# Kernel tuning notes

Measured on AMD Instinct MI355X. Metric: run time of the kernel, lower is better.

## Reference

```python
import jax, jax.numpy as jnp
import numpy as np

N_NODES = 50000


def _relgraphconv(x, W, Wloop, b, src, dst, etypes, n_nodes):
    # DGL RelGraphConv (regularizer=None, self_loop=True, norm=None):
    # out[i] = sum over incoming edges (j->i, rel r) of W_r @ x[j]  +  W_loop @ x[i]  +  b
    # low-mem form: transform all nodes per relation, then gather per edge.
    h_rel = jnp.einsum('ni,rio->rno', x, W)          # [R, N, out]
    msg = h_rel[etypes, src]                          # [E, out]
    agg = jax.ops.segment_sum(msg, dst, num_segments=n_nodes)  # [N, out]
    return agg + x @ Wloop + b


def setup_inputs() -> dict:
    key = jax.random.key(0)
    ks = jax.random.split(key, 12)
    N, E, n_state = N_NODES, 800000, 128
    inp = {
        'x': jax.random.normal(ks[0], (N, n_state), dtype=jnp.float32),
        'src': jax.random.randint(ks[1], (E,), 0, N, dtype=jnp.int32),
        'dst': jax.random.randint(ks[2], (E,), 0, N, dtype=jnp.int32),
        'etypes': jax.random.randint(ks[3], (E,), 0, 2, dtype=jnp.int32),
        'cell_size': jax.random.randint(ks[4], (N,), 0, 8, dtype=jnp.int32),
        'max_size': jax.random.randint(ks[5], (N,), 0, 8, dtype=jnp.int32),
        'W1': jax.random.normal(ks[6], (2, n_state, 64), dtype=jnp.float32) * 0.05,
        'loop1': jax.random.normal(ks[7], (n_state, 64), dtype=jnp.float32) * 0.05,
        'b1': jnp.zeros((64,), dtype=jnp.float32),
        'W2': jax.random.normal(ks[8], (2, 64, 64), dtype=jnp.float32) * 0.05,
        'loop2': jax.random.normal(ks[9], (64, 64), dtype=jnp.float32) * 0.05,
        'b2': jnp.zeros((64,), dtype=jnp.float32),
        'W3': jax.random.normal(ks[10], (2, 64, 2), dtype=jnp.float32) * 0.05,
        'loop3': jax.random.normal(ks[11], (64, 2), dtype=jnp.float32) * 0.05,
        'b3': jnp.zeros((2,), dtype=jnp.float32),
    }
    return inp


def reference(x, src, dst, etypes, cell_size, max_size,
              W1, loop1, b1, W2, loop2, b2, W3, loop3, b3):
    N = x.shape[0]
    h = jax.nn.relu(_relgraphconv(x, W1, loop1, b1, src, dst, etypes, N))
    h = jax.nn.relu(_relgraphconv(h, W2, loop2, b2, src, dst, etypes, N))
    h = _relgraphconv(h, W3, loop3, b3, src, dst, etypes, N)   # [N, 2]
    # action mask: col 0 = cannot upsize, col 1 = cannot downsize
    upper = cell_size >= (max_size - 1)
    lower = cell_size == 0
    mask = jnp.stack([upper, lower], axis=1)                   # [N, 2] bool
    return jnp.where(mask, h.min() - 1.0, h)
```

## Files before the change

### kernel.cpp

```cpp
#include <hip/hip_runtime.h>


#define STRIDE 64
#define BINCAP 2560

typedef unsigned short ushortT;
typedef __attribute__((ext_vector_type(8))) short short8;
typedef __attribute__((ext_vector_type(4))) float f32x4;

__device__ inline ushortT f2bf(float f) {
    union { float f; unsigned u; } v; v.f = f;
    unsigned r = v.u + 0x7FFFu + ((v.u >> 16) & 1u);
    return (ushortT)(r >> 16);
}
__device__ inline float bf2f(ushortT h) {
    union { unsigned u; float f; } v; v.u = ((unsigned)h) << 16;
    return v.f;
}

__device__ inline void atomicMinF(float* addr, float v) {
    if (v >= 0.f) atomicMin((int*)addr, __float_as_int(v));
    else          atomicMax((unsigned int*)addr, __float_as_uint(v));
}

__global__ __launch_bounds__(256) void pack_init_kernel(
    const float* __restrict__ W1, const float* __restrict__ loop1,
    const float* __restrict__ W2, const float* __restrict__ loop2,
    ushortT* __restrict__ BP1, ushortT* __restrict__ BP2,
    int* __restrict__ bincnt, float* __restrict__ minval, int NBINS) {
    int g = (int)blockIdx.x * 256 + (int)threadIdx.x;
    if (g < NBINS) bincnt[g] = 0;
    if (g == 0) *(int*)minval = 0x7f7f7f7f;
    if (g < 3072) {
        int l = g & 63, ks = (g >> 6) & 3, ct = g >> 8;
        int c = ct * 16 + (l & 15);
        int mat = c >> 6, cc = c & 63;
        int kbase = ks * 32 + (l >> 4) * 8;
        ushortT* dstp = BP1 + (size_t)g * 8;
#pragma unroll
        for (int j = 0; j < 8; ++j) {
            int k = kbase + j;
            float v = (mat < 2) ? W1[((size_t)mat * 128 + k) * 64 + cc]
                                : loop1[(size_t)k * 64 + cc];
            dstp[j] = f2bf(v);
        }
    } else {
        int s = g - 3072;
        int l = s & 63;
        int ks = (s >> 6) % 6;
        int ct = s / 384;
        int c = ct * 16 + (l & 15);
        int kbase = ks * 32 + (l >> 4) * 8;
        ushortT* dstp = BP2 + (size_t)s * 8;
#pragma unroll
        for (int j = 0; j < 8; ++j) {
            int k = kbase + j;
            float v = (k < 128) ? W2[(size_t)k * 64 + c]
                                : loop2[(size_t)(k - 128) * 64 + c];
            dstp[j] = f2bf(v);
        }
    }
}

__global__ __launch_bounds__(256) void k1_kernel(
    const float* __restrict__ x, const ushortT* __restrict__ BP1,
    const float* __restrict__ b1,
    ushortT* __restrict__ hrelb, ushortT* __restrict__ H1b,
    const int* __restrict__ src, const int* __restrict__ dst,
    const int* __restrict__ et, int* __restrict__ bincnt, int2* __restrict__ binbuf,
    int N, int E, int NBINS, int NBA) {
    __shared__ int hist[512];
    __shared__ int gbase[512];
    __shared__ ushortT rnk[4096];

    const int t = (int)threadIdx.x;

    if ((int)blockIdx.x < NBA) {
        for (int i = t; i < NBINS; i += 256) hist[i] = 0;
        __syncthreads();
        const int base = (int)blockIdx.x * 4096;
#pragma unroll
        for (int i = 0; i < 16; ++i) {
            int e = base + t + i * 256;
            if (e < E) {
                int bb = dst[e] >> 7;
                rnk[t + i * 256] = (ushortT)atomicAdd(&hist[bb], 1);
            }
        }
        __syncthreads();
        for (int i = t; i < NBINS; i += 256) {
            int h = hist[i];
            gbase[i] = h ? atomicAdd(&bincnt[i], h) : 0;
        }
        __syncthreads();
#pragma unroll
        for (int i = 0; i < 16; ++i) {
            int e = base + t + i * 256;
            if (e < E) {
                int dd = dst[e];
                int bb = dd >> 7;
                int v = et[e] * N + src[e];
                int pos = gbase[bb] + (int)rnk[t + i * 256];
                if (pos < BINCAP)
                    binbuf[(size_t)bb * BINCAP + pos] = make_int2(dd, v);
            }
        }
        return;
    }
    const int w = t >> 6, lane = t & 63;
    const int rowbase = (((int)blockIdx.x - NBA) * 4 + w) * 16;
    const int m = lane & 15, quad = lane >> 4;
    const int nclamp = min(rowbase + m, N - 1);

    short8 a[4];
    const float* xp = x + (size_t)nclamp * 128 + quad * 8;
#pragma unroll
    for (int ks = 0; ks < 4; ++ks) {
        float4 g0 = *(const float4*)(xp + ks * 32);
        float4 g1 = *(const float4*)(xp + ks * 32 + 4);
        a[ks][0] = (short)f2bf(g0.x); a[ks][1] = (short)f2bf(g0.y);
        a[ks][2] = (short)f2bf(g0.z); a[ks][3] = (short)f2bf(g0.w);
        a[ks][4] = (short)f2bf(g1.x); a[ks][5] = (short)f2bf(g1.y);
        a[ks][6] = (short)f2bf(g1.z); a[ks][7] = (short)f2bf(g1.w);
    }

    f32x4 acc[12];
#pragma unroll
    for (int ct = 0; ct < 12; ++ct) acc[ct] = (f32x4){0.f, 0.f, 0.f, 0.f};

#pragma unroll
    for (int ks = 0; ks < 4; ++ks) {
#pragma unroll
        for (int ct = 0; ct < 12; ++ct) {
            short8 b = *(const short8*)&BP1[((size_t)(ct * 4 + ks) * 64 + lane) * 8];
            acc[ct] = __builtin_amdgcn_mfma_f32_16x16x32_bf16(a[ks], b, acc[ct], 0, 0, 0);
        }
    }

    const int node0 = rowbase + quad * 4;
#pragma unroll
    for (int ct = 0; ct < 12; ++ct) {
        int c = ct * 16 + m;
        int mat = c >> 6, cc = c & 63;
        float bias = (mat == 2) ? b1[cc] : 0.f;
#pragma unroll
        for (int j = 0; j < 4; ++j) {
            int n = node0 + j;
            if (n < N) {
                float v = acc[ct][j] + bias;
                if (mat < 2) hrelb[((size_t)mat * N + n) * 64 + cc] = f2bf(v);
                else         H1b[(size_t)n * 64 + cc] = f2bf(v);
            }
        }
    }
}

__global__ __launch_bounds__(256) void phaseB_kernel(
    const int* __restrict__ bincnt, const int2* __restrict__ binbuf,
    int* __restrict__ cnt, int* __restrict__ eidx, int N) {
    __shared__ int lcnt[128];
    const int b = (int)blockIdx.x;
    const int t = (int)threadIdx.x;
    if (t < 128) lcnt[t] = 0;
    __syncthreads();
    const int cb = min(bincnt[b], BINCAP);
    const int2* buf = binbuf + (size_t)b * BINCAP;
    for (int i = t; i < cb; i += 256) {
        int2 rec = buf[i];
        int r = atomicAdd(&lcnt[rec.x & 127], 1);
        if (r < STRIDE) eidx[(size_t)rec.x * STRIDE + r] = rec.y;
    }
    __syncthreads();
    int node = b * 128 + t;
    if (t < 128 && node < N) cnt[node] = min(lcnt[t], STRIDE);
}

__device__ __forceinline__ float gather_accum(
    const ushortT* __restrict__ hb, int my, int deg, int lane, float acc) {
    for (int j = 0; j < deg; j += 16) {
        float v[16];
#pragma unroll
        for (int q = 0; q < 16; ++q) {
            int jj = j + q;
            int sel = (jj < deg) ? jj : 0;
            int id = __shfl(my, sel, 64);
            float wgt = (jj < deg) ? 1.f : 0.f;
            v[q] = wgt * bf2f(hb[(size_t)id * 64 + lane]);
        }
        float s0 = (v[0] + v[1]) + (v[2] + v[3]);
        float s1 = (v[4] + v[5]) + (v[6] + v[7]);
        float s2 = (v[8] + v[9]) + (v[10] + v[11]);
        float s3 = (v[12] + v[13]) + (v[14] + v[15]);
        acc += (s0 + s1) + (s2 + s3);
    }
    return acc;
}

__global__ void agg1_kernel(const ushortT* __restrict__ hrelb, const int* __restrict__ eidx,
                            const int* __restrict__ cnt, ushortT* __restrict__ H1b, int N) {
    int node = (int)blockIdx.x * 4 + ((int)threadIdx.x >> 6);
    if (node >= N) return;
    int lane = (int)threadIdx.x & 63;
    int deg = cnt[node];
    int my = (lane < deg) ? eidx[(size_t)node * STRIDE + lane] : 0;
    float acc = bf2f(H1b[(size_t)node * 64 + lane]);
    acc = gather_accum(hrelb, my, deg, lane, acc);
    H1b[(size_t)node * 64 + lane] = f2bf(fmaxf(acc, 0.f));
}

__global__ void agg2_kernel(const ushortT* __restrict__ H1b, const int* __restrict__ eidx,
                            const int* __restrict__ cnt, ushortT* __restrict__ Sb, int N) {
    int node = (int)blockIdx.x * 4 + ((int)threadIdx.x >> 6);
    if (node >= N) return;
    int lane = (int)threadIdx.x & 63;
    int deg = cnt[node];
    int my = (lane < deg) ? eidx[(size_t)node * STRIDE + lane] : 0;
    float a0 = 0.f, a1 = 0.f;
    for (int j = 0; j < deg; j += 16) {
        float v[16], w0[16], w1[16];
#pragma unroll
        for (int q = 0; q < 16; ++q) {
            int jj = j + q;
            int sel = (jj < deg) ? jj : 0;
            int id = __shfl(my, sel, 64);
            int rel = (id >= N) ? 1 : 0;
            int row = id - rel * N;
            float live = (jj < deg) ? 1.f : 0.f;
            w0[q] = rel ? 0.f : live;
            w1[q] = rel ? live : 0.f;
            v[q] = bf2f(H1b[(size_t)row * 64 + lane]);
        }
#pragma unroll
        for (int q = 0; q < 16; ++q) {
            a0 += w0[q] * v[q];
            a1 += w1[q] * v[q];
        }
    }
    Sb[(size_t)node * 64 + lane] = f2bf(a0);
    Sb[((size_t)N + node) * 64 + lane] = f2bf(a1);
}

__global__ __launch_bounds__(256) void gemm23_kernel(
    const ushortT* __restrict__ Sb, const ushortT* __restrict__ H1b,
    const ushortT* __restrict__ BP2, const float* __restrict__ b2,
    const float* __restrict__ W3, const float* __restrict__ loop3,
    const float* __restrict__ b3,
    float* __restrict__ hrel3, float* __restrict__ H3, int N) {
    const int w = (int)threadIdx.x >> 6, lane = (int)threadIdx.x & 63;
    const int rowbase = ((int)blockIdx.x * 4 + w) * 16;
    const int m = lane & 15, quad = lane >> 4;
    const int nclamp = min(rowbase + m, N - 1);

    f32x4 acc[4];
#pragma unroll
    for (int ct = 0; ct < 4; ++ct) acc[ct] = (f32x4){0.f, 0.f, 0.f, 0.f};

#pragma unroll
    for (int ks = 0; ks < 6; ++ks) {
        const ushortT* base =
            (ks < 2) ? (Sb + (size_t)nclamp * 64)
          : (ks < 4) ? (Sb + ((size_t)N + nclamp) * 64)
                     : (H1b + (size_t)nclamp * 64);
        short8 a = *(const short8*)(base + (ks & 1) * 32 + quad * 8);
#pragma unroll
        for (int ct = 0; ct < 4; ++ct) {
            short8 b = *(const short8*)&BP2[((size_t)(ct * 6 + ks) * 64 + lane) * 8];
            acc[ct] = __builtin_amdgcn_mfma_f32_16x16x32_bf16(a, b, acc[ct], 0, 0, 0);
        }
    }

    float h2[4][4];
#pragma unroll
    for (int ct = 0; ct < 4; ++ct) {
        float bias = b2[ct * 16 + m];
#pragma unroll
        for (int j = 0; j < 4; ++j) h2[ct][j] = fmaxf(acc[ct][j] + bias, 0.f);
    }

    float w3v[4][6];
#pragma unroll
    for (int ct = 0; ct < 4; ++ct) {
        int k = ct * 16 + m;
        w3v[ct][0] = W3[k * 2 + 0];
        w3v[ct][1] = W3[k * 2 + 1];
        w3v[ct][2] = W3[(64 + k) * 2 + 0];
        w3v[ct][3] = W3[(64 + k) * 2 + 1];
        w3v[ct][4] = loop3[k * 2 + 0];
        w3v[ct][5] = loop3[k * 2 + 1];
    }
    float p[4][6];
#pragma unroll
    for (int j = 0; j < 4; ++j)
#pragma unroll
        for (int c = 0; c < 6; ++c) p[j][c] = 0.f;
#pragma unroll
    for (int j = 0; j < 4; ++j)
#pragma unroll
        for (int ct = 0; ct < 4; ++ct)
#pragma unroll
            for (int c = 0; c < 6; ++c) p[j][c] += h2[ct][j] * w3v[ct][c];

#pragma unroll
    for (int mask = 1; mask <= 8; mask <<= 1) {
#pragma unroll
        for (int j = 0; j < 4; ++j)
#pragma unroll
            for (int c = 0; c < 6; ++c) p[j][c] += __shfl_xor(p[j][c], mask, 64);
    }

    if (m == 0) {
#pragma unroll
        for (int j = 0; j < 4; ++j) {
            int n = rowbase + quad * 4 + j;
            if (n < N) {
                hrel3[(size_t)n * 2 + 0] = p[j][0];
                hrel3[(size_t)n * 2 + 1] = p[j][1];
                hrel3[((size_t)N + n) * 2 + 0] = p[j][2];
                hrel3[((size_t)N + n) * 2 + 1] = p[j][3];
                H3[(size_t)n * 2 + 0] = p[j][4] + b3[0];
                H3[(size_t)n * 2 + 1] = p[j][5] + b3[1];
            }
        }
    }
}

__global__ void agg3min_kernel(const float* __restrict__ hrel3, const int* __restrict__ eidx,
                               const int* __restrict__ cnt, float* __restrict__ H3,
                               float* __restrict__ minval, int N) {
    int n = (int)blockIdx.x * 256 + (int)threadIdx.x;
    float v = 3.4e38f;
    if (n < N) {
        float a0 = H3[n * 2 + 0], a1 = H3[n * 2 + 1];
        int deg = cnt[n];
        const int* row = &eidx[(size_t)n * STRIDE];
        for (int j = 0; j < deg; j += 8) {
            float2 q[8];
            float wg[8];
#pragma unroll
            for (int qq = 0; qq < 8; ++qq) {
                int jj = j + qq;
                int sel = (jj < deg) ? jj : 0;
                int idx = row[sel];
                wg[qq] = (jj < deg) ? 1.f : 0.f;
                q[qq] = *(const float2*)&hrel3[(size_t)idx * 2];
            }
#pragma unroll
            for (int qq = 0; qq < 8; ++qq) {
                a0 += wg[qq] * q[qq].x;
                a1 += wg[qq] * q[qq].y;
            }
        }
        H3[n * 2 + 0] = a0;
        H3[n * 2 + 1] = a1;
        v = fminf(a0, a1);
    }
#pragma unroll
    for (int mm = 32; mm >= 1; mm >>= 1) v = fminf(v, __shfl_xor(v, mm, 64));
    __shared__ float s[4];
    if ((threadIdx.x & 63) == 0) s[threadIdx.x >> 6] = v;
    __syncthreads();
    if (threadIdx.x == 0)
        atomicMinF(minval, fminf(fminf(s[0], s[1]), fminf(s[2], s[3])));
}

__global__ void mask_kernel(const float* __restrict__ H3, const float* __restrict__ minval,
                            const int* __restrict__ cs, const int* __restrict__ ms,
                            float* __restrict__ out, int N) {
    int n = (int)blockIdx.x * 256 + (int)threadIdx.x;
    if (n >= N) return;
    float m = minval[0] - 1.0f;
    bool up = cs[n] >= ms[n] - 1;
    bool lo = cs[n] == 0;
    out[n * 2 + 0] = up ? m : H3[n * 2 + 0];
    out[n * 2 + 1] = lo ? m : H3[n * 2 + 1];
}

extern "C" void kernel_launch(void* const* d_in, const int* in_sizes, int n_in,
                              void* d_out, int out_size, void* d_ws, size_t ws_size,
                              hipStream_t stream) {
    const float* x     = (const float*)d_in[0];
    const int* src     = (const int*)d_in[1];
    const int* dst     = (const int*)d_in[2];
    const int* etypes  = (const int*)d_in[3];
    const int* cellsz  = (const int*)d_in[4];
    const int* maxsz   = (const int*)d_in[5];
    const float* W1    = (const float*)d_in[6];
    const float* loop1 = (const float*)d_in[7];
    const float* b1    = (const float*)d_in[8];
    const float* W2    = (const float*)d_in[9];
    const float* loop2 = (const float*)d_in[10];
    const float* b2    = (const float*)d_in[11];
    const float* W3    = (const float*)d_in[12];
    const float* loop3 = (const float*)d_in[13];
    const float* b3    = (const float*)d_in[14];
    float* out = (float*)d_out;

    const int N = in_sizes[0] / 128;
    const int E = in_sizes[1];

    char* p = (char*)d_ws;
    auto alloc = [&](size_t bytes) -> void* {
        void* r = (void*)p;
        p += ((bytes + 255) / 256) * 256;
        return r;
    };
    ushortT* hrelb  = (ushortT*)alloc((size_t)2 * N * 64 * 2);
    ushortT* H1b    = (ushortT*)alloc((size_t)N * 64 * 2);
    ushortT* Sb     = (ushortT*)alloc((size_t)2 * N * 64 * 2);
    float* hrel3    = (float*)alloc((size_t)2 * N * 2 * 4);
    float* H3       = (float*)alloc((size_t)N * 2 * 4);
    int* cnt        = (int*)alloc((size_t)N * 4);
    int* eidx       = (int*)alloc((size_t)N * STRIDE * 4);
    ushortT* BP1    = (ushortT*)alloc((size_t)3072 * 8 * 2);
    ushortT* BP2    = (ushortT*)alloc((size_t)1536 * 8 * 2);
    float* minval   = (float*)alloc(4);

    const int NBINS = (N + 127) >> 7;
    int* bincnt     = (int*)alloc((size_t)NBINS * 4);
    int2* binbuf    = (int2*)alloc((size_t)NBINS * BINCAP * 8);
    (void)ws_size; (void)n_in; (void)out_size;

    const int NB_N   = (N + 255) / 256;
    const int NTILES = (N + 63) / 64;
    const int NB_W   = (N + 3) / 4;
    const int NBA    = (E + 4095) / 4096;

    pack_init_kernel<<<18, 256, 0, stream>>>(
        W1, loop1, W2, loop2, BP1, BP2, bincnt, minval, NBINS);

    k1_kernel<<<NBA + NTILES, 256, 0, stream>>>(
        x, BP1, b1, hrelb, H1b,
        src, dst, etypes, bincnt, binbuf, N, E, NBINS, NBA);

    phaseB_kernel<<<NBINS, 256, 0, stream>>>(bincnt, binbuf, cnt, eidx, N);

    agg1_kernel<<<NB_W, 256, 0, stream>>>(hrelb, eidx, cnt, H1b, N);

    agg2_kernel<<<NB_W, 256, 0, stream>>>(H1b, eidx, cnt, Sb, N);

    gemm23_kernel<<<NTILES, 256, 0, stream>>>(Sb, H1b, BP2, b2, W3, loop3, b3,
                                              hrel3, H3, N);

    agg3min_kernel<<<NB_N, 256, 0, stream>>>(hrel3, eidx, cnt, H3, minval, N);
    mask_kernel<<<NB_N, 256, 0, stream>>>(H3, minval, cellsz, maxsz, out, N);
}
```

Before: 218.6 us.

## Regroup prologue kernels: fuse weight packing with binning, GEMM1 with bin scatter

Reorganizes the first three launches. Weight packing now shares a launch with edge binning (phase A), and the layer-1 GEMM shares a launch with the per-node scatter of binned edges (phase B), using a block-index split in each. The bincnt zeroing moves to a hipMemsetAsync. This cuts one kernel launch and lets the independent GEMM work overlap the phase-B scatter. The cost is an extra memset call, and phase-B blocks now carry the GEMM kernel's register footprint.

```diff
diff --git a/kernel.cpp b/kernel.cpp
--- a/kernel.cpp
+++ b/kernel.cpp
@@ -23,92 +23,112 @@
     else          atomicMax((unsigned int*)addr, __float_as_uint(v));
 }
 
-__global__ __launch_bounds__(256) void pack_init_kernel(
+__global__ __launch_bounds__(256) void pack_phaseA_kernel(
     const float* __restrict__ W1, const float* __restrict__ loop1,
     const float* __restrict__ W2, const float* __restrict__ loop2,
     ushortT* __restrict__ BP1, ushortT* __restrict__ BP2,
-    int* __restrict__ bincnt, float* __restrict__ minval, int NBINS) {
-    int g = (int)blockIdx.x * 256 + (int)threadIdx.x;
-    if (g < NBINS) bincnt[g] = 0;
-    if (g == 0) *(int*)minval = 0x7f7f7f7f;
-    if (g < 3072) {
-        int l = g & 63, ks = (g >> 6) & 3, ct = g >> 8;
-        int c = ct * 16 + (l & 15);
-        int mat = c >> 6, cc = c & 63;
-        int kbase = ks * 32 + (l >> 4) * 8;
-        ushortT* dstp = BP1 + (size_t)g * 8;
-#pragma unroll
-        for (int j = 0; j < 8; ++j) {
-            int k = kbase + j;
-            float v = (mat < 2) ? W1[((size_t)mat * 128 + k) * 64 + cc]
-                                : loop1[(size_t)k * 64 + cc];
-            dstp[j] = f2bf(v);
-        }
-    } else {
-        int s = g - 3072;
-        int l = s & 63;
-        int ks = (s >> 6) % 6;
-        int ct = s / 384;
-        int c = ct * 16 + (l & 15);
-        int kbase = ks * 32 + (l >> 4) * 8;
-        ushortT* dstp = BP2 + (size_t)s * 8;
-#pragma unroll
-        for (int j = 0; j < 8; ++j) {
-            int k = kbase + j;
-            float v = (k < 128) ? W2[(size_t)k * 64 + c]
-                                : loop2[(size_t)(k - 128) * 64 + c];
-            dstp[j] = f2bf(v);
-        }
-    }
-}
-
-__global__ __launch_bounds__(256) void k1_kernel(
+    float* __restrict__ minval,
+    const int* __restrict__ src, const int* __restrict__ dst,
+    const int* __restrict__ et, int* __restrict__ bincnt, int2* __restrict__ binbuf,
+    int N, int E, int NBINS) {
+    __shared__ int hist[512];
+    __shared__ int gbase[512];
+    __shared__ ushortT rnk[4096];
+    const int t = (int)threadIdx.x;
+
+    if ((int)blockIdx.x < 18) {
+        int g = (int)blockIdx.x * 256 + t;
+        if (g == 0) *(int*)minval = 0x7f7f7f7f;
+        if (g < 3072) {
+            int l = g & 63, ks = (g >> 6) & 3, ct = g >> 8;
+            int c = ct * 16 + (l & 15);
+            int mat = c >> 6, cc = c & 63;
+            int kbase = ks * 32 + (l >> 4) * 8;
+            ushortT* dstp = BP1 + (size_t)g * 8;
+#pragma unroll
+            for (int j = 0; j < 8; ++j) {
+                int k = kbase + j;
+                float v = (mat < 2) ? W1[((size_t)mat * 128 + k) * 64 + cc]
+                                    : loop1[(size_t)k * 64 + cc];
+                dstp[j] = f2bf(v);
+            }
+        } else {
+            int s = g - 3072;
+            int l = s & 63;
+            int ks = (s >> 6) % 6;
+            int ct = s / 384;
+            int c = ct * 16 + (l & 15);
+            int kbase = ks * 32 + (l >> 4) * 8;
+            ushortT* dstp = BP2 + (size_t)s * 8;
+#pragma unroll
+            for (int j = 0; j < 8; ++j) {
+                int k = kbase + j;
+                float v = (k < 128) ? W2[(size_t)k * 64 + c]
+                                    : loop2[(size_t)(k - 128) * 64 + c];
+                dstp[j] = f2bf(v);
+            }
+        }
+        return;
+    }
+    for (int i = t; i < NBINS; i += 256) hist[i] = 0;
+    __syncthreads();
+    const int base = ((int)blockIdx.x - 18) * 4096;
+#pragma unroll
+    for (int i = 0; i < 16; ++i) {
+        int e = base + t + i * 256;
+        if (e < E) {
+            int bb = dst[e] >> 7;
+            rnk[t + i * 256] = (ushortT)atomicAdd(&hist[bb], 1);
+        }
+    }
+    __syncthreads();
+    for (int i = t; i < NBINS; i += 256) {
+        int h = hist[i];
+        gbase[i] = h ? atomicAdd(&bincnt[i], h) : 0;
+    }
+    __syncthreads();
+#pragma unroll
+    for (int i = 0; i < 16; ++i) {
+        int e = base + t + i * 256;
+        if (e < E) {
+            int dd = dst[e];
+            int bb = dd >> 7;
+            int v = et[e] * N + src[e];
+            int pos = gbase[bb] + (int)rnk[t + i * 256];
+            if (pos < BINCAP)
+                binbuf[(size_t)bb * BINCAP + pos] = make_int2(dd, v);
+        }
+    }
+}
+
+__global__ __launch_bounds__(256) void gemm1_phaseB_kernel(
     const float* __restrict__ x, const ushortT* __restrict__ BP1,
     const float* __restrict__ b1,
     ushortT* __restrict__ hrelb, ushortT* __restrict__ H1b,
-    const int* __restrict__ src, const int* __restrict__ dst,
-    const int* __restrict__ et, int* __restrict__ bincnt, int2* __restrict__ binbuf,
-    int N, int E, int NBINS, int NBA) {
-    __shared__ int hist[512];
-    __shared__ int gbase[512];
-    __shared__ ushortT rnk[4096];
-
+    const int* __restrict__ bincnt, const int2* __restrict__ binbuf,
+    int* __restrict__ cnt, int* __restrict__ eidx,
+    int N, int NBINS) {
+    __shared__ int lcnt[128];
     const int t = (int)threadIdx.x;
 
-    if ((int)blockIdx.x < NBA) {
-        for (int i = t; i < NBINS; i += 256) hist[i] = 0;
+    if ((int)blockIdx.x < NBINS) {
+        const int b = (int)blockIdx.x;
+        if (t < 128) lcnt[t] = 0;
         __syncthreads();
-        const int base = (int)blockIdx.x * 4096;
-#pragma unroll
-        for (int i = 0; i < 16; ++i) {
-            int e = base + t + i * 256;
-            if (e < E) {
-                int bb = dst[e] >> 7;
-                rnk[t + i * 256] = (ushortT)atomicAdd(&hist[bb], 1);
-            }
+        const int cb = min(bincnt[b], BINCAP);
+        const int2* buf = binbuf + (size_t)b * BINCAP;
+        for (int i = t; i < cb; i += 256) {
+            int2 rec = buf[i];
+            int r = atomicAdd(&lcnt[rec.x & 127], 1);
+            if (r < STRIDE) eidx[(size_t)rec.x * STRIDE + r] = rec.y;
         }
         __syncthreads();
-        for (int i = t; i < NBINS; i += 256) {
-            int h = hist[i];
-            gbase[i] = h ? atomicAdd(&bincnt[i], h) : 0;
-        }
-        __syncthreads();
-#pragma unroll
-        for (int i = 0; i < 16; ++i) {
-            int e = base + t + i * 256;
-            if (e < E) {
-                int dd = dst[e];
-                int bb = dd >> 7;
-                int v = et[e] * N + src[e];
-                int pos = gbase[bb] + (int)rnk[t + i * 256];
-                if (pos < BINCAP)
-                    binbuf[(size_t)bb * BINCAP + pos] = make_int2(dd, v);
-            }
-        }
+        int node = b * 128 + t;
+        if (t < 128 && node < N) cnt[node] = min(lcnt[t], STRIDE);
         return;
     }
     const int w = t >> 6, lane = t & 63;
-    const int rowbase = (((int)blockIdx.x - NBA) * 4 + w) * 16;
+    const int rowbase = (((int)blockIdx.x - NBINS) * 4 + w) * 16;
     const int m = lane & 15, quad = lane >> 4;
     const int nclamp = min(rowbase + m, N - 1);
 
@@ -153,26 +173,6 @@
             }
         }
     }
-}
-
-__global__ __launch_bounds__(256) void phaseB_kernel(
-    const int* __restrict__ bincnt, const int2* __restrict__ binbuf,
-    int* __restrict__ cnt, int* __restrict__ eidx, int N) {
-    __shared__ int lcnt[128];
-    const int b = (int)blockIdx.x;
-    const int t = (int)threadIdx.x;
-    if (t < 128) lcnt[t] = 0;
-    __syncthreads();
-    const int cb = min(bincnt[b], BINCAP);
-    const int2* buf = binbuf + (size_t)b * BINCAP;
-    for (int i = t; i < cb; i += 256) {
-        int2 rec = buf[i];
-        int r = atomicAdd(&lcnt[rec.x & 127], 1);
-        if (r < STRIDE) eidx[(size_t)rec.x * STRIDE + r] = rec.y;
-    }
-    __syncthreads();
-    int node = b * 128 + t;
-    if (t < 128 && node < N) cnt[node] = min(lcnt[t], STRIDE);
 }
 
 __device__ __forceinline__ float gather_accum(
@@ -425,14 +425,14 @@
     const int NB_W   = (N + 3) / 4;
     const int NBA    = (E + 4095) / 4096;
 
-    pack_init_kernel<<<18, 256, 0, stream>>>(
-        W1, loop1, W2, loop2, BP1, BP2, bincnt, minval, NBINS);
-
-    k1_kernel<<<NBA + NTILES, 256, 0, stream>>>(
-        x, BP1, b1, hrelb, H1b,
-        src, dst, etypes, bincnt, binbuf, N, E, NBINS, NBA);
-
-    phaseB_kernel<<<NBINS, 256, 0, stream>>>(bincnt, binbuf, cnt, eidx, N);
+    hipMemsetAsync(bincnt, 0, (size_t)NBINS * 4, stream);
+
+    pack_phaseA_kernel<<<18 + NBA, 256, 0, stream>>>(
+        W1, loop1, W2, loop2, BP1, BP2, minval,
+        src, dst, etypes, bincnt, binbuf, N, E, NBINS);
+
+    gemm1_phaseB_kernel<<<NBINS + NTILES, 256, 0, stream>>>(
+        x, BP1, b1, hrelb, H1b, bincnt, binbuf, cnt, eidx, N, NBINS);
 
     agg1_kernel<<<NB_W, 256, 0, stream>>>(hrelb, eidx, cnt, H1b, N);
 
@@ -442,5 +442,6 @@
                                               hrel3, H3, N);
 
     agg3min_kernel<<<NB_N, 256, 0, stream>>>(hrel3, eidx, cnt, H3, minval, N);
+
     mask_kernel<<<NB_N, 256, 0, stream>>>(H3, minval, cellsz, maxsz, out, N);
 }
```

After: 223.2 us. 1.02x slower.
